# Performance work log

Hardware: AMD Instinct MI355X
Metric: run time of the kernel (lower is better)

## Reference

```python
import jax, jax.numpy as jnp
import numpy as np

N, E, D, H, K = 8192, 8, 1024, 4096, 2


def setup_inputs() -> dict:
    key = jax.random.key(0)
    ks = jax.random.split(key, 12)
    s = 0.02  # init scale for weights
    return {
        "x": jax.random.normal(ks[0], (N, D), jnp.float32),
        "noise": jax.random.normal(ks[1], (N, E), jnp.float32),
        "Wg_w": jax.random.normal(ks[2], (D, E), jnp.float32) * s,
        "Wg_b": jnp.zeros((E,), jnp.float32),
        "Wn_w": jax.random.normal(ks[3], (D, E), jnp.float32) * s,
        "Wn_b": jnp.zeros((E,), jnp.float32),
        "w1": jax.random.normal(ks[4], (E, D, H), jnp.float32) * s,
        "b1": jnp.zeros((E, H), jnp.float32),
        "w2": jax.random.normal(ks[5], (E, H, D), jnp.float32) * s,
        "b2": jnp.zeros((E, D), jnp.float32),
        "k": K,
    }


def reference(x, noise, Wg_w, Wg_b, Wn_w, Wn_b, w1, b1, w2, b2, k):
    # --- noisy top-k gating: H(x) = Wg(x) + noise * softplus(Wn(x)) ---
    g_logits = x @ Wg_w + Wg_b                       # [N, E]
    n_scale = jax.nn.softplus(x @ Wn_w + Wn_b)       # [N, E]
    h = g_logits + noise * n_scale                   # [N, E]
    topk_vals, topk_inds = jax.lax.top_k(h, k)       # [N, k]
    gates = jax.nn.softmax(topk_vals, axis=-1)       # [N, k]

    # Scatter top-k gates into a dense [N, E] map (zeros for unselected experts),
    # so the weighted combine is exactly sum_j gates[n,j] * expert_{inds[n,j]}(x_n).
    n_tok, n_exp = h.shape
    dense_gates = jnp.zeros((n_tok, n_exp), h.dtype).at[
        jnp.arange(n_tok)[:, None], topk_inds
    ].set(gates)                                     # [N, E]

    # --- per-expert 2-layer MLP: fc2(relu(fc1(x))) ---
    hid = jax.nn.relu(jnp.einsum('nd,edh->neh', x, w1) + b1)  # [N, E, H]
    y = jnp.einsum('neh,ehd->ned', hid, w2) + b2              # [N, E, D]
    out = jnp.einsum('ned,ne->nd', y, dense_gates)            # [N, D]
    return out
```

## Files before the change

### kernel.cpp

```cpp
#include <hip/hip_runtime.h>
#include <hip/hip_bf16.h>

#define NTOK 8192
#define NEXP 8
#define DMODEL 1024
#define DHID 4096

typedef __bf16 bf16x8 __attribute__((ext_vector_type(8)));
typedef float f32x4 __attribute__((ext_vector_type(4)));

__device__ __forceinline__ unsigned short f2bf(float f) {
  return __builtin_bit_cast(unsigned short, __float2bfloat16(f));
}

__device__ __forceinline__ void gload_lds16(const void* g, void* l) {
  __builtin_amdgcn_global_load_lds(
      (const __attribute__((address_space(1))) unsigned int*)g,
      (__attribute__((address_space(3))) unsigned int*)l, 16, 0, 0);
}

__device__ __forceinline__ int imin(int a, int b) { return a < b ? a : b; }

constexpr size_t OFF_XB   = 0;
constexpr size_t OFF_W1T  = OFF_XB + (size_t)NTOK * DMODEL * 2;
constexpr size_t OFF_W2T  = OFF_W1T + (size_t)NEXP * DHID * DMODEL * 2;
constexpr size_t OFF_HID  = OFF_W2T + (size_t)NEXP * DMODEL * DHID * 2;
constexpr size_t OFF_IDX  = OFF_HID + (size_t)NTOK * 2 * DHID * 2;
constexpr size_t OFF_GATE = OFF_IDX + (size_t)NTOK * 2 * 4;
constexpr size_t OFF_LIST = OFF_GATE + (size_t)NTOK * 2 * 4;
constexpr size_t OFF_CNT  = OFF_LIST + (size_t)NTOK * 2 * 4;
constexpr size_t OFF_OFFS = OFF_CNT + 128;
constexpr size_t OFF_CUR  = OFF_OFFS + 128;

__global__ __launch_bounds__(256) void prep_kernel(
    const float* __restrict__ w1, const float* __restrict__ w2,
    unsigned short* __restrict__ w1t, unsigned short* __restrict__ w2t,
    const float* __restrict__ x, const float* __restrict__ noise,
    const float* __restrict__ Wg_w, const float* __restrict__ Wg_b,
    const float* __restrict__ Wn_w, const float* __restrict__ Wn_b,
    unsigned short* __restrict__ xb, int* __restrict__ topk_idx,
    float* __restrict__ topk_gate, int* __restrict__ counts) {
  __shared__ float sh[64][65];
  const int bid = blockIdx.x;

  if (bid < 16384) {
    const float* in;
    unsigned short* outp;
    int R, C, r0, c0;
    if (bid < 8192) {
      int e = bid >> 10, rem = bid & 1023;
      R = DMODEL; C = DHID;
      in = w1 + (size_t)e * R * C;
      outp = w1t + (size_t)e * R * C;
      r0 = (rem >> 6) * 64;
      c0 = (rem & 63) * 64;
    } else {
      int t = bid - 8192;
      int e = t >> 10, rem = t & 1023;
      R = DHID; C = DMODEL;
      in = w2 + (size_t)e * R * C;
      outp = w2t + (size_t)e * R * C;
      r0 = (rem >> 4) * 64;
      c0 = (rem & 15) * 64;
    }
    int tx = threadIdx.x & 15, ty = threadIdx.x >> 4;
#pragma unroll
    for (int p = 0; p < 4; ++p) {
      int row = ty + p * 16;
      float4 v = *(const float4*)&in[(size_t)(r0 + row) * C + c0 + tx * 4];
      sh[row][tx * 4 + 0] = v.x;
      sh[row][tx * 4 + 1] = v.y;
      sh[row][tx * 4 + 2] = v.z;
      sh[row][tx * 4 + 3] = v.w;
    }
    __syncthreads();
#pragma unroll
    for (int p = 0; p < 4; ++p) {
      int crow = ty + p * 16;
      ushort4 o;
      o.x = f2bf(sh[tx * 4 + 0][crow]);
      o.y = f2bf(sh[tx * 4 + 1][crow]);
      o.z = f2bf(sh[tx * 4 + 2][crow]);
      o.w = f2bf(sh[tx * 4 + 3][crow]);
      *(ushort4*)&outp[(size_t)(c0 + crow) * R + r0 + tx * 4] = o;
    }
    return;
  }

  int g = bid - 16384;
  int wave = threadIdx.x >> 6;
  int lane = threadIdx.x & 63;
  int n = g * 4 + wave;
  if (n >= NTOK) return;

  float ag[8] = {0.f, 0.f, 0.f, 0.f, 0.f, 0.f, 0.f, 0.f};
  float an[8] = {0.f, 0.f, 0.f, 0.f, 0.f, 0.f, 0.f, 0.f};
  const float* xr = x + (size_t)n * DMODEL;
  unsigned short* xbr = xb + (size_t)n * DMODEL;
#pragma unroll 4
  for (int i = 0; i < DMODEL / 64; ++i) {
    int d = lane + i * 64;
    float xv = xr[d];
    xbr[d] = f2bf(xv);
    const float4* wg = (const float4*)(Wg_w + (size_t)d * 8);
    const float4* wn = (const float4*)(Wn_w + (size_t)d * 8);
    float4 g0 = wg[0], g1 = wg[1];
    float4 n0 = wn[0], n1 = wn[1];
    ag[0] += xv * g0.x; ag[1] += xv * g0.y; ag[2] += xv * g0.z; ag[3] += xv * g0.w;
    ag[4] += xv * g1.x; ag[5] += xv * g1.y; ag[6] += xv * g1.z; ag[7] += xv * g1.w;
    an[0] += xv * n0.x; an[1] += xv * n0.y; an[2] += xv * n0.z; an[3] += xv * n0.w;
    an[4] += xv * n1.x; an[5] += xv * n1.y; an[6] += xv * n1.z; an[7] += xv * n1.w;
  }
#pragma unroll
  for (int off = 32; off > 0; off >>= 1) {
#pragma unroll
    for (int j = 0; j < 8; ++j) {
      ag[j] += __shfl_down(ag[j], off, 64);
      an[j] += __shfl_down(an[j], off, 64);
    }
  }
  if (lane == 0) {
    float h[8];
#pragma unroll
    for (int e = 0; e < 8; ++e) {
      float gl = ag[e] + Wg_b[e];
      float z = an[e] + Wn_b[e];
      float sp = fmaxf(z, 0.f) + log1pf(expf(-fabsf(z)));
      h[e] = gl + noise[(size_t)n * 8 + e] * sp;
    }
    int i0 = 0; float v0 = h[0];
#pragma unroll
    for (int e = 1; e < 8; ++e)
      if (h[e] > v0) { v0 = h[e]; i0 = e; }
    int i1 = -1; float v1 = -1e30f;
#pragma unroll
    for (int e = 0; e < 8; ++e)
      if (e != i0 && h[e] > v1) { v1 = h[e]; i1 = e; }
    float e1 = expf(v1 - v0);
    float inv = 1.f / (1.f + e1);
    topk_idx[n * 2] = i0;
    topk_idx[n * 2 + 1] = i1;
    topk_gate[n * 2] = inv;
    topk_gate[n * 2 + 1] = e1 * inv;
    atomicAdd(&counts[i0], 1);
    atomicAdd(&counts[i1], 1);
  }
}

__global__ void scan_kernel(const int* __restrict__ counts,
                            int* __restrict__ offsets, int* __restrict__ cursor) {
  if (threadIdx.x == 0) {
    int acc = 0;
    for (int e = 0; e < NEXP; ++e) {
      offsets[e] = acc;
      cursor[e] = acc;
      acc += counts[e];
    }
    offsets[NEXP] = acc;
  }
}

__global__ void scatter_kernel(const int* __restrict__ topk_idx,
                               int* __restrict__ cursor, int* __restrict__ list) {
  int n = blockIdx.x * 256 + threadIdx.x;
  if (n >= NTOK) return;
#pragma unroll
  for (int j = 0; j < 2; ++j) {
    int e = topk_idx[n * 2 + j];
    int pos = atomicAdd(&cursor[e], 1);
    list[pos] = n * 2 + j;
  }
}

#define VMW(N) asm volatile("s_waitcnt vmcnt(" #N ")" ::: "memory")

template <int MODE>
__global__ __launch_bounds__(256, 4) void expert_gemm(
    const unsigned short* __restrict__ Asrc, const unsigned short* __restrict__ Bt,
    const float* __restrict__ bias, const int* __restrict__ offsets,
    const int* __restrict__ list, const float* __restrict__ gates,
    unsigned short* __restrict__ hid, float* __restrict__ out) {
  constexpr int Krow = MODE ? DHID : DMODEL;
  constexpr int Nout = MODE ? DMODEL : DHID;
  constexpr int NT = Krow / 32;

  const int gx = gridDim.x, gy = gridDim.y;
  const int lin = blockIdx.x + gx * (blockIdx.y + gy * blockIdx.z);
  const int e = lin & 7;
  int r = lin >> 3;

  int by, bx;
  if (MODE == 0) {
    int st = r >> 6;
    int inner = r & 63;
    int sm = st >> 2, sn = st & 3;
    if (sm & 1) sn = 3 - sn;
    by = sm * 8 + (inner >> 3);
    bx = sn * 8 + (inner & 7);
  } else {
    by = r & 63;
    bx = r >> 6;
  }

  const int off = offsets[e];
  const int ne = offsets[e + 1] - off;
  const int m0 = by * 128;
  if (m0 >= ne) return;
  const int n0 = bx * 128;

  __shared__ alignas(16) unsigned short Al[3][128 * 32];
  __shared__ alignas(16) unsigned short Bl[3][128 * 32];

  const int tid = threadIdx.x;
  const int lane = tid & 63;
  const int w = tid >> 6;
  const int wm = (w >> 1) * 64;
  const int wn = (w & 1) * 64;
  const int lr = lane & 15;
  const int kg = lane >> 4;
  const int chrd = (kg ^ ((lr >> 1) & 3)) * 8;

  const unsigned short* srcA[2];
  const unsigned short* srcB[2];
#pragma unroll
  for (int i = 0; i < 2; ++i) {
    int q = tid + i * 256;
    int rr = q >> 2, c = q & 3;
    int cs = c ^ ((rr >> 1) & 3);
    int p = off + imin(m0 + rr, ne - 1);
    if (MODE == 0) {
      int token = list[p] >> 1;
      srcA[i] = Asrc + (size_t)token * DMODEL + cs * 8;
    } else {
      srcA[i] = Asrc + (size_t)p * DHID + cs * 8;
    }
    srcB[i] = Bt + (size_t)e * Nout * Krow + (size_t)(n0 + rr) * Krow + cs * 8;
  }

  f32x4 acc[4][4] = {};

  auto stage = [&](int slot, int kt) {
#pragma unroll
    for (int i = 0; i < 2; ++i) {
      int q = tid + i * 256;
      gload_lds16(srcA[i] + kt * 32, &Al[slot][q * 8]);
      gload_lds16(srcB[i] + kt * 32, &Bl[slot][q * 8]);
    }
  };

  auto compute = [&](int slot) {
    bf16x8 af[4], bfr[4];
#pragma unroll
    for (int mf = 0; mf < 4; ++mf)
      af[mf] = *(const bf16x8*)&Al[slot][(wm + mf * 16 + lr) * 32 + chrd];
#pragma unroll
    for (int nf = 0; nf < 4; ++nf)
      bfr[nf] = *(const bf16x8*)&Bl[slot][(wn + nf * 16 + lr) * 32 + chrd];
    asm volatile("s_waitcnt lgkmcnt(0)" ::: "memory");
    __builtin_amdgcn_sched_barrier(0);
    if (MODE == 1) __builtin_amdgcn_s_setprio(1);
#pragma unroll
    for (int mf = 0; mf < 4; ++mf)
#pragma unroll
      for (int nf = 0; nf < 4; ++nf)
        acc[mf][nf] = __builtin_amdgcn_mfma_f32_16x16x32_bf16(af[mf], bfr[nf],
                                                              acc[mf][nf], 0, 0, 0);
    if (MODE == 1) __builtin_amdgcn_s_setprio(0);
  };

  stage(0, 0);
  stage(1, 1);
  stage(2, 2);

  int cur = 0;
  for (int t = 0; t < NT; ++t) {
    if (t < NT - 2) { VMW(8); }
    else if (t == NT - 2) { VMW(4); }
    else { VMW(0); }
    __builtin_amdgcn_s_barrier();
    __builtin_amdgcn_sched_barrier(0);
    compute(cur);
    asm volatile("s_waitcnt lgkmcnt(0)" ::: "memory");
    __builtin_amdgcn_sched_barrier(0);
    __builtin_amdgcn_s_barrier();
    if (t + 3 < NT) stage(cur, t + 3);
    cur = (cur == 2) ? 0 : cur + 1;
  }

  if (MODE == 0) {
#pragma unroll
    for (int mf = 0; mf < 4; ++mf) {
#pragma unroll
      for (int j = 0; j < 4; ++j) {
        int rloc = wm + mf * 16 + kg * 4 + j;
        int row = m0 + rloc;
        if (row < ne) {
          size_t p = (size_t)(off + row);
#pragma unroll
          for (int nf = 0; nf < 4; ++nf) {
            int col = n0 + wn + nf * 16 + lr;
            float v = acc[mf][nf][j] + bias[(size_t)e * Nout + col];
            hid[p * DHID + col] = f2bf(fmaxf(v, 0.f));
          }
        }
      }
    }
  } else {
#pragma unroll
    for (int mf = 0; mf < 4; ++mf) {
#pragma unroll
      for (int j = 0; j < 4; ++j) {
        int rloc = wm + mf * 16 + kg * 4 + j;
        int row = m0 + rloc;
        if (row < ne) {
          int lv = list[off + row];
          int token = lv >> 1;
          float g = gates[lv];
#pragma unroll
          for (int nf = 0; nf < 4; ++nf) {
            int col = n0 + wn + nf * 16 + lr;
            float v = (acc[mf][nf][j] + bias[(size_t)e * Nout + col]) * g;
            atomicAdd(&out[(size_t)token * DMODEL + col], v);
          }
        }
      }
    }
  }
}

extern "C" void kernel_launch(void* const* d_in, const int* in_sizes, int n_in,
                              void* d_out, int out_size, void* d_ws, size_t ws_size,
                              hipStream_t stream) {
  const float* x = (const float*)d_in[0];
  const float* noise = (const float*)d_in[1];
  const float* Wg_w = (const float*)d_in[2];
  const float* Wg_b = (const float*)d_in[3];
  const float* Wn_w = (const float*)d_in[4];
  const float* Wn_b = (const float*)d_in[5];
  const float* w1 = (const float*)d_in[6];
  const float* b1 = (const float*)d_in[7];
  const float* w2 = (const float*)d_in[8];
  const float* b2 = (const float*)d_in[9];
  float* out = (float*)d_out;

  char* ws = (char*)d_ws;
  unsigned short* xb = (unsigned short*)(ws + OFF_XB);
  unsigned short* w1t = (unsigned short*)(ws + OFF_W1T);
  unsigned short* w2t = (unsigned short*)(ws + OFF_W2T);
  unsigned short* hid = (unsigned short*)(ws + OFF_HID);
  int* topk_idx = (int*)(ws + OFF_IDX);
  float* topk_gate = (float*)(ws + OFF_GATE);
  int* list = (int*)(ws + OFF_LIST);
  int* counts = (int*)(ws + OFF_CNT);
  int* offsets = (int*)(ws + OFF_OFFS);
  int* cursor = (int*)(ws + OFF_CUR);

  hipMemsetAsync(out, 0, (size_t)NTOK * DMODEL * sizeof(float), stream);
  hipMemsetAsync(counts, 0, NEXP * sizeof(int), stream);

  prep_kernel<<<18432, 256, 0, stream>>>(w1, w2, w1t, w2t, x, noise, Wg_w, Wg_b,
                                         Wn_w, Wn_b, xb, topk_idx, topk_gate,
                                         counts);
  scan_kernel<<<1, 64, 0, stream>>>(counts, offsets, cursor);
  scatter_kernel<<<NTOK / 256, 256, 0, stream>>>(topk_idx, cursor, list);

  expert_gemm<0><<<dim3(32, 64, NEXP), 256, 0, stream>>>(
      xb, w1t, b1, offsets, list, topk_gate, hid, nullptr);
  expert_gemm<1><<<dim3(8, 64, NEXP), 256, 0, stream>>>(
      hid, w2t, b2, offsets, list, topk_gate, nullptr, out);
}
```

Measured before the change: 829.5 us.

## Enlarge expert GEMM M-tile to 256 rows with 128x64 warp tiles

Doubles the per-block row tile of both expert GEMMs from 128 to 256, giving each wave a 128x64 accumulator tile, so each B (weight) tile loaded into LDS is reused across twice as many token rows. The grid y-dimension is halved to match, the swizzled/grouped block ordering for the first GEMM is replaced by a plain column-major mapping, and the MODE 1 priority toggling is removed. The cost is double the accumulator registers and A-side LDS, with launch bounds lowered to 2 blocks per CU, which reduces occupancy. Partially filled 256-row tiles waste more work at expert boundaries.

```diff
diff --git a/kernel.cpp b/kernel.cpp
--- a/kernel.cpp
+++ b/kernel.cpp
@@ -175,7 +175,7 @@
 #define VMW(N) asm volatile("s_waitcnt vmcnt(" #N ")" ::: "memory")
 
 template <int MODE>
-__global__ __launch_bounds__(256, 4) void expert_gemm(
+__global__ __launch_bounds__(256, 2) void expert_gemm(
     const unsigned short* __restrict__ Asrc, const unsigned short* __restrict__ Bt,
     const float* __restrict__ bias, const int* __restrict__ offsets,
     const int* __restrict__ list, const float* __restrict__ gates,
@@ -187,46 +187,37 @@
   const int gx = gridDim.x, gy = gridDim.y;
   const int lin = blockIdx.x + gx * (blockIdx.y + gy * blockIdx.z);
   const int e = lin & 7;
-  int r = lin >> 3;
-
-  int by, bx;
-  if (MODE == 0) {
-    int st = r >> 6;
-    int inner = r & 63;
-    int sm = st >> 2, sn = st & 3;
-    if (sm & 1) sn = 3 - sn;
-    by = sm * 8 + (inner >> 3);
-    bx = sn * 8 + (inner & 7);
-  } else {
-    by = r & 63;
-    bx = r >> 6;
-  }
+  const int r = lin >> 3;
+  const int by = r % gy;
+  const int bx = r / gy;
 
   const int off = offsets[e];
   const int ne = offsets[e + 1] - off;
-  const int m0 = by * 128;
+  const int m0 = by * 256;
   if (m0 >= ne) return;
   const int n0 = bx * 128;
 
-  __shared__ alignas(16) unsigned short Al[3][128 * 32];
+  __shared__ alignas(16) unsigned short Al[3][256 * 32];
   __shared__ alignas(16) unsigned short Bl[3][128 * 32];
 
   const int tid = threadIdx.x;
   const int lane = tid & 63;
   const int w = tid >> 6;
-  const int wm = (w >> 1) * 64;
+  const int wm = (w >> 1) * 128;
   const int wn = (w & 1) * 64;
   const int lr = lane & 15;
   const int kg = lane >> 4;
   const int chrd = (kg ^ ((lr >> 1) & 3)) * 8;
 
-  const unsigned short* srcA[2];
+  const unsigned short* srcA[4];
   const unsigned short* srcB[2];
-#pragma unroll
-  for (int i = 0; i < 2; ++i) {
+  int qa[4], qb[2];
+#pragma unroll
+  for (int i = 0; i < 4; ++i) {
     int q = tid + i * 256;
     int rr = q >> 2, c = q & 3;
     int cs = c ^ ((rr >> 1) & 3);
+    qa[i] = q;
     int p = off + imin(m0 + rr, ne - 1);
     if (MODE == 0) {
       int token = list[p] >> 1;
@@ -234,38 +225,43 @@
     } else {
       srcA[i] = Asrc + (size_t)p * DHID + cs * 8;
     }
+  }
+#pragma unroll
+  for (int i = 0; i < 2; ++i) {
+    int q = tid + i * 256;
+    int rr = q >> 2, c = q & 3;
+    int cs = c ^ ((rr >> 1) & 3);
+    qb[i] = q;
     srcB[i] = Bt + (size_t)e * Nout * Krow + (size_t)(n0 + rr) * Krow + cs * 8;
   }
 
-  f32x4 acc[4][4] = {};
+  f32x4 acc[8][4] = {};
 
   auto stage = [&](int slot, int kt) {
 #pragma unroll
-    for (int i = 0; i < 2; ++i) {
-      int q = tid + i * 256;
-      gload_lds16(srcA[i] + kt * 32, &Al[slot][q * 8]);
-      gload_lds16(srcB[i] + kt * 32, &Bl[slot][q * 8]);
-    }
+    for (int i = 0; i < 4; ++i)
+      gload_lds16(srcA[i] + kt * 32, &Al[slot][qa[i] * 8]);
+#pragma unroll
+    for (int i = 0; i < 2; ++i)
+      gload_lds16(srcB[i] + kt * 32, &Bl[slot][qb[i] * 8]);
   };
 
   auto compute = [&](int slot) {
-    bf16x8 af[4], bfr[4];
-#pragma unroll
-    for (int mf = 0; mf < 4; ++mf)
+    bf16x8 af[8], bfr[4];
+#pragma unroll
+    for (int mf = 0; mf < 8; ++mf)
       af[mf] = *(const bf16x8*)&Al[slot][(wm + mf * 16 + lr) * 32 + chrd];
 #pragma unroll
     for (int nf = 0; nf < 4; ++nf)
       bfr[nf] = *(const bf16x8*)&Bl[slot][(wn + nf * 16 + lr) * 32 + chrd];
     asm volatile("s_waitcnt lgkmcnt(0)" ::: "memory");
     __builtin_amdgcn_sched_barrier(0);
-    if (MODE == 1) __builtin_amdgcn_s_setprio(1);
-#pragma unroll
-    for (int mf = 0; mf < 4; ++mf)
+#pragma unroll
+    for (int mf = 0; mf < 8; ++mf)
 #pragma unroll
       for (int nf = 0; nf < 4; ++nf)
         acc[mf][nf] = __builtin_amdgcn_mfma_f32_16x16x32_bf16(af[mf], bfr[nf],
                                                               acc[mf][nf], 0, 0, 0);
-    if (MODE == 1) __builtin_amdgcn_s_setprio(0);
   };
 
   stage(0, 0);
@@ -274,8 +270,8 @@
 
   int cur = 0;
   for (int t = 0; t < NT; ++t) {
-    if (t < NT - 2) { VMW(8); }
-    else if (t == NT - 2) { VMW(4); }
+    if (t < NT - 2) { VMW(12); }
+    else if (t == NT - 2) { VMW(6); }
     else { VMW(0); }
     __builtin_amdgcn_s_barrier();
     __builtin_amdgcn_sched_barrier(0);
@@ -289,7 +285,7 @@
 
   if (MODE == 0) {
 #pragma unroll
-    for (int mf = 0; mf < 4; ++mf) {
+    for (int mf = 0; mf < 8; ++mf) {
 #pragma unroll
       for (int j = 0; j < 4; ++j) {
         int rloc = wm + mf * 16 + kg * 4 + j;
@@ -307,7 +303,7 @@
     }
   } else {
 #pragma unroll
-    for (int mf = 0; mf < 4; ++mf) {
+    for (int mf = 0; mf < 8; ++mf) {
 #pragma unroll
       for (int j = 0; j < 4; ++j) {
         int rloc = wm + mf * 16 + kg * 4 + j;
@@ -364,8 +360,8 @@
   scan_kernel<<<1, 64, 0, stream>>>(counts, offsets, cursor);
   scatter_kernel<<<NTOK / 256, 256, 0, stream>>>(topk_idx, cursor, list);
 
-  expert_gemm<0><<<dim3(32, 64, NEXP), 256, 0, stream>>>(
+  expert_gemm<0><<<dim3(DHID / 128, 32, NEXP), 256, 0, stream>>>(
       xb, w1t, b1, offsets, list, topk_gate, hid, nullptr);
-  expert_gemm<1><<<dim3(8, 64, NEXP), 256, 0, stream>>>(
+  expert_gemm<1><<<dim3(DMODEL / 128, 32, NEXP), 256, 0, stream>>>(
       hid, w2t, b2, offsets, list, topk_gate, nullptr, out);
 }
```

Result: slower. 968.8 us (+16.8%).
